# Optimization experiments

Hardware: AMD Instinct MI355X
Metric: run time of the kernel (lower is better)

Reference implementation:

```python
import jax, jax.numpy as jnp
import numpy as np
from jax import lax

B, N, S, C_IN, C_OUT = 4, 16384, 4096, 256, 256


def setup_inputs() -> dict:
    key = jax.random.key(0)
    k1, k2, k3, k4 = jax.random.split(key, 4)
    xyz1 = jax.random.normal(k1, (B, 3, N), dtype=jnp.float32)
    xyz2 = jax.random.normal(k2, (B, 3, S), dtype=jnp.float32)
    points2 = jax.random.normal(k3, (B, C_IN, S), dtype=jnp.float32)
    W = jax.random.normal(k4, (C_OUT, C_IN), dtype=jnp.float32) * (1.0 / np.sqrt(C_IN))
    b = jnp.zeros((C_OUT,), dtype=jnp.float32)
    return {"xyz1": xyz1, "xyz2": xyz2, "points2": points2, "W": W, "b": b}


def reference(xyz1, xyz2, points2, W, b):
    # channel-first -> channel-last
    p1 = jnp.transpose(xyz1, (0, 2, 1))        # [B, N, 3]
    p2 = jnp.transpose(xyz2, (0, 2, 1))        # [B, S, 3]
    f2 = jnp.transpose(points2, (0, 2, 1))     # [B, S, C]
    Bn, Nn, _ = p1.shape
    Cn = f2.shape[-1]
    # squared pairwise distances [B, N, S]
    d = (-2.0 * jnp.einsum('bnc,bsc->bns', p1, p2)
         + jnp.sum(p1 * p1, axis=-1)[:, :, None]
         + jnp.sum(p2 * p2, axis=-1)[:, None, :])
    # 3 nearest neighbors (smallest distances) -- equivalent to sort + slice :3
    neg_d3, idx = lax.top_k(-d, 3)             # [B, N, 3]
    d3 = -neg_d3
    recip = 1.0 / (d3 + 1e-8)
    weight = recip / jnp.sum(recip, axis=-1, keepdims=True)   # [B, N, 3]
    # gather neighbor features: [B, N, 3, C]
    gathered = jnp.take_along_axis(
        f2, idx.reshape(Bn, Nn * 3)[..., None], axis=1
    ).reshape(Bn, Nn, 3, Cn)
    interp = jnp.sum(gathered * weight[..., None], axis=2)    # [B, N, C]
    # Conv1d(kernel=1) == per-point linear: [B, C_out, N]
    out = jnp.einsum('bnc,oc->bon', interp, W) + b[None, :, None]
    return out
```

## Files before the change

### kernel.cpp

```cpp
#include <hip/hip_runtime.h>

#define BB 4
#define NN 16384
#define SS 4096
#define CIN 256
#define COUT 256

#define SC 8
#define SCS (SS / SC)
#define SUBS 16
#define SUBL 256
#define KNNB ((NN / 512) * SC * BB)
#define GEMMB ((COUT / 64) * (SS / 64) * BB)
#define RSLVB (BB * NN / 4)

typedef float v2f __attribute__((ext_vector_type(2)));
typedef float v4f __attribute__((ext_vector_type(4)));

__device__ __forceinline__ unsigned short f2bf(float f) {
    unsigned u = __float_as_uint(f);
    u += 0x7FFF + ((u >> 16) & 1);
    return (unsigned short)(u >> 16);
}
__device__ __forceinline__ float bf2f(unsigned short h) {
    return __uint_as_float((unsigned)h << 16);
}

__device__ __forceinline__ void ins_v(float e, float& a, float& b, float& c) {
    float n1 = __builtin_amdgcn_fmed3f(e, a, b);
    float n2 = __builtin_amdgcn_fmed3f(e, b, c);
    a = fminf(a, e); b = n1; c = n2;
}

__device__ __forceinline__ void insert_vi(float e, int gi,
                                          float& k0, float& k1, float& k2,
                                          int& i0, int& i1, int& i2) {
    bool c0 = e < k0, c1 = e < k1, c2 = e < k2;
    float n0 = fminf(e, k0);
    float n1 = __builtin_amdgcn_fmed3f(e, k0, k1);
    float n2 = __builtin_amdgcn_fmed3f(e, k1, k2);
    int t1 = c0 ? i0 : gi;
    int t2 = c1 ? i1 : gi;
    i0 = c0 ? gi : i0;
    i1 = c1 ? t1 : i1;
    i2 = c2 ? t2 : i2;
    k0 = n0; k1 = n1; k2 = n2;
}

__device__ __forceinline__ void ins_lex(float e, int gi,
                                        float& k0, float& k1, float& k2,
                                        int& i0, int& i1, int& i2) {
    bool c0 = (e < k0) || (e == k0 && gi < i0);
    bool c1 = (e < k1) || (e == k1 && gi < i1);
    bool c2 = (e < k2) || (e == k2 && gi < i2);
    float n0 = fminf(e, k0);
    float n1 = __builtin_amdgcn_fmed3f(e, k0, k1);
    float n2 = __builtin_amdgcn_fmed3f(e, k1, k2);
    int t1 = c0 ? i0 : gi;
    int t2 = c1 ? i1 : gi;
    i0 = c0 ? gi : i0;
    i1 = c1 ? t1 : i1;
    i2 = c2 ? t2 : i2;
    k0 = n0; k1 = n1; k2 = n2;
}

__device__ __forceinline__ int ltc(unsigned long long m) {
    return __builtin_amdgcn_mbcnt_hi(
        (unsigned)(m >> 32), __builtin_amdgcn_mbcnt_lo((unsigned)m, 0));
}

#define E2_FROM(p_xy, p_zw, XX, YY, ZZ, e2)                                    \
    do {                                                                       \
        asm("v_pk_fma_f32 %0, %1, %2, %3 op_sel:[0,0,1] op_sel_hi:[0,1,1]"     \
            : "=v"(e2) : "v"(p_zw), "v"(ZZ), "v"(p_zw));                       \
        asm("v_pk_fma_f32 %0, %1, %2, %0 op_sel:[1,0,0] op_sel_hi:[1,1,1]"     \
            : "+v"(e2) : "v"(p_xy), "v"(YY));                                  \
        asm("v_pk_fma_f32 %0, %1, %2, %0 op_sel:[0,0,0] op_sel_hi:[0,1,1]"     \
            : "+v"(e2) : "v"(p_xy), "v"(XX));                                  \
    } while (0)

#define PK_LO(acc, ap, bw)                                                     \
    asm("v_pk_fma_f32 %0, %1, %2, %0 op_sel:[0,0,0] op_sel_hi:[0,1,1]"         \
        : "+v"(acc) : "v"(ap), "v"(bw))
#define PK_HI(acc, ap, bw)                                                     \
    asm("v_pk_fma_f32 %0, %1, %2, %0 op_sel:[1,0,0] op_sel_hi:[1,1,1]"         \
        : "+v"(acc) : "v"(ap), "v"(bw))

__device__ __forceinline__ void knn_phase(int id, int t, float* smem,
                                          const float* __restrict__ xyz1,
                                          const float* __restrict__ xyz2,
                                          float* __restrict__ pv,
                                          float4* __restrict__ cand4) {
    int nb = id & 31;
    int ch = (id >> 5) & 7;
    int b  = id >> 8;
    int s0 = ch * SCS;

    float4* smv = (float4*)smem;
    const float* x2 = xyz2 + (size_t)b * 3 * SS;
    for (int i = t; i < SCS; i += 256) {
        float px = x2[s0 + i];
        float py = x2[SS + s0 + i];
        float pz = x2[2 * SS + s0 + i];
        float4 p4 = make_float4(px, py, pz, fmaf(px, px, fmaf(py, py, pz * pz)));
        smv[i] = p4;
        if (nb == 0) cand4[(size_t)b * SS + s0 + i] = p4;
    }
    __syncthreads();

    int n0  = nb * 512 + t;
    int n1q = n0 + 256;
    const float* xb = xyz1 + (size_t)b * 3 * NN;
    float ax = xb[n0],  ay = xb[NN + n0],  az = xb[2 * NN + n0];
    float bx = xb[n1q], by = xb[NN + n1q], bz = xb[2 * NN + n1q];
    v2f XX = {-2.0f * ax, -2.0f * bx};
    v2f YY = {-2.0f * ay, -2.0f * by};
    v2f ZZ = {-2.0f * az, -2.0f * bz};

#pragma unroll
    for (int half = 0; half < 2; ++half) {
        float A0 = 1e30f, A1 = 1e30f, A2 = 1e30f;
        float B0 = 1e30f, B1 = 1e30f, B2 = 1e30f;
        int sb = half * SUBL;
#pragma unroll 8
        for (int s = sb; s < sb + SUBL; ++s) {
            v4f p = *(const v4f*)(smem + 4 * s);
            v2f pxy = __builtin_shufflevector(p, p, 0, 1);
            v2f pzw = __builtin_shufflevector(p, p, 2, 3);
            v2f e2;
            E2_FROM(pxy, pzw, XX, YY, ZZ, e2);
            float nA1 = __builtin_amdgcn_fmed3f(e2.x, A0, A1);
            float nA2 = __builtin_amdgcn_fmed3f(e2.x, A1, A2);
            A0 = fminf(A0, e2.x); A1 = nA1; A2 = nA2;
            float nB1 = __builtin_amdgcn_fmed3f(e2.y, B0, B1);
            float nB2 = __builtin_amdgcn_fmed3f(e2.y, B1, B2);
            B0 = fminf(B0, e2.y); B1 = nB1; B2 = nB2;
        }
        int sub = ch * 2 + half;
        size_t base = (size_t)(sub * BB + b) * 3;
        pv[(base + 0) * NN + n0]  = A0;
        pv[(base + 1) * NN + n0]  = A1;
        pv[(base + 2) * NN + n0]  = A2;
        pv[(base + 0) * NN + n1q] = B0;
        pv[(base + 1) * NN + n1q] = B1;
        pv[(base + 2) * NN + n1q] = B2;
    }
}

__device__ __forceinline__ void gemm_phase(int g, int t, float* smem,
                                           const float* __restrict__ P,
                                           const float* __restrict__ W,
                                           const float* __restrict__ bias,
                                           unsigned short* __restrict__ Gh) {
    int o0 = (g & 3) * 64;
    int s0 = ((g >> 2) & 63) * 64;
    int b  = g >> 8;
    float* sP = smem;
    float* sW = smem + 1024;
    int i = t & 15;
    int j = t >> 4;

    v2f acc2[4][2];
#pragma unroll
    for (int p = 0; p < 4; ++p) {
        acc2[p][0] = (v2f){0.f, 0.f};
        acc2[p][1] = (v2f){0.f, 0.f};
    }

    const float* Pb = P + (size_t)b * CIN * SS;

    for (int c0 = 0; c0 < CIN; c0 += 16) {
        __syncthreads();
        {
            int col = t & 63;
            int r0r = t >> 6;
#pragma unroll
            for (int r = 0; r < 4; ++r) {
                int row = r0r + r * 4;
                sP[row * 64 + col] = Pb[(size_t)(c0 + row) * SS + s0 + col];
            }
        }
        {
            int cc = t & 15;
            int obase = t >> 4;
#pragma unroll
            for (int r = 0; r < 4; ++r) {
                int oo = obase + 16 * r;
                sW[cc * 68 + oo] = W[(size_t)(o0 + oo) * CIN + c0 + cc];
            }
        }
        __syncthreads();

#pragma unroll
        for (int cc = 0; cc < 16; ++cc) {
            v4f a  = *(const v4f*)&sP[cc * 64 + i * 4];
            v4f bv = *(const v4f*)&sW[cc * 68 + j * 4];
            v2f a01 = __builtin_shufflevector(a, a, 0, 1);
            v2f a23 = __builtin_shufflevector(a, a, 2, 3);
            v2f b01 = __builtin_shufflevector(bv, bv, 0, 1);
            v2f b23 = __builtin_shufflevector(bv, bv, 2, 3);
            PK_LO(acc2[0][0], a01, b01); PK_LO(acc2[0][1], a01, b23);
            PK_HI(acc2[1][0], a01, b01); PK_HI(acc2[1][1], a01, b23);
            PK_LO(acc2[2][0], a23, b01); PK_LO(acc2[2][1], a23, b23);
            PK_HI(acc2[3][0], a23, b01); PK_HI(acc2[3][1], a23, b23);
        }
    }

    float b0 = bias[o0 + j * 4 + 0];
    float b1 = bias[o0 + j * 4 + 1];
    float b2 = bias[o0 + j * 4 + 2];
    float b3 = bias[o0 + j * 4 + 3];
#pragma unroll
    for (int p = 0; p < 4; ++p) {
        ushort4 v;
        v.x = f2bf(acc2[p][0].x + b0);
        v.y = f2bf(acc2[p][0].y + b1);
        v.z = f2bf(acc2[p][1].x + b2);
        v.w = f2bf(acc2[p][1].y + b3);
        size_t off = ((size_t)b * SS + s0 + i * 4 + p) * COUT + o0 + j * 4;
        *(ushort4*)&Gh[off] = v;
    }
}

__global__ __launch_bounds__(256) void k_fused(const float* __restrict__ xyz1,
                                               const float* __restrict__ xyz2,
                                               const float* __restrict__ P,
                                               const float* __restrict__ W,
                                               const float* __restrict__ bias,
                                               unsigned short* __restrict__ Gh,
                                               float* __restrict__ pv,
                                               float4* __restrict__ cand4) {
    __shared__ float smem[2112];
    int bid = blockIdx.x;
    int t   = threadIdx.x;

    if (bid < KNNB) {
        knn_phase(bid, t, smem, xyz1, xyz2, pv, cand4);
    } else {
        gemm_phase(bid - KNNB, t, smem, P, W, bias, Gh);
    }
}

__global__ __launch_bounds__(256) void k_resolve(const float* __restrict__ pv,
                                                 const float* __restrict__ xyz1,
                                                 const float4* __restrict__ cand4,
                                                 float4* __restrict__ wi4,
                                                 int4* __restrict__ gi4) {
    __shared__ uint2 sl[4][16];
    int t   = threadIdx.x;
    int wid = t >> 6;
    int l   = t & 63;
    int g   = blockIdx.x * 4 + wid;
    int b   = g >> 14;
    int n   = g & (NN - 1);

    float ov = 1e30f;
    if (l < 48)
        ov = pv[(size_t)(((l & 15) * BB + b) * 3 + (l >> 4)) * NN + n];
    float m0 = ov, m1 = 1e30f, m2 = 1e30f;
#pragma unroll
    for (int xm = 1; xm < 64; xm <<= 1) {
        float s0 = __shfl_xor(m0, xm);
        float s1 = __shfl_xor(m1, xm);
        float s2 = __shfl_xor(m2, xm);
        ins_v(s0, m0, m1, m2);
        ins_v(s1, m0, m1, m2);
        ins_v(s2, m0, m1, m2);
    }

    unsigned mm = (unsigned)__ballot((l < 16) && (ov <= m2)) & 0xFFFFu;

    const float* xb = xyz1 + (size_t)b * 3 * NN;
    float qx = xb[n], qy = xb[NN + n], qz = xb[2 * NN + n];
    float xm2c = -2.0f * qx, ym2c = -2.0f * qy, zm2c = -2.0f * qz;
    const float4* cb = cand4 + (size_t)b * SS;

    float k0 = 1e30f, k1 = 1e30f, k2 = 1e30f;
    int   i0 = 0,     i1 = 0,     i2 = 0;
    unsigned msc = mm;
    while (msc) {
        int sub = __builtin_ctz(msc); msc &= msc - 1;
        int sb = sub * SUBL;
#pragma unroll
        for (int r = 0; r < 4; ++r) {
            int gi = sb + r * 64 + l;
            float4 p = cb[gi];
            float e = fmaf(p.x, xm2c, fmaf(p.y, ym2c, fmaf(p.z, zm2c, p.w)));
            insert_vi(e, gi, k0, k1, k2, i0, i1, i2);
        }
    }

    unsigned long long b0 = __ballot(k0 <= m2);
    unsigned long long b1 = __ballot(k1 <= m2);
    unsigned long long b2 = __ballot(k2 <= m2);
    int p0 = __popcll(b0), p1 = __popcll(b1);
    int cnt3 = p0 + p1 + __popcll(b2);
    if (cnt3 <= 16) {
        if (k0 <= m2) sl[wid][ltc(b0)]           = make_uint2(__float_as_uint(k0), (unsigned)i0);
        if (k1 <= m2) sl[wid][p0 + ltc(b1)]      = make_uint2(__float_as_uint(k1), (unsigned)i1);
        if (k2 <= m2) sl[wid][p0 + p1 + ltc(b2)] = make_uint2(__float_as_uint(k2), (unsigned)i2);
    }
    __syncthreads();

    float K0 = 1e30f, K1 = 1e30f, K2 = 1e30f;
    int   I0 = 0,     I1 = 0,     I2 = 0;
    if (cnt3 <= 16) {
        for (int j = 0; j < cnt3; ++j) {
            uint2 u = sl[wid][j];
            ins_lex(__uint_as_float(u.x), (int)u.y, K0, K1, K2, I0, I1, I2);
        }
    } else {
        unsigned mf = mm;
        while (mf) {
            int sub = __builtin_ctz(mf); mf &= mf - 1;
            int sb = sub * SUBL;
            for (int s = 0; s < SUBL; ++s) {
                float4 p = cb[sb + s];
                float e = fmaf(p.x, xm2c, fmaf(p.y, ym2c, fmaf(p.z, zm2c, p.w)));
                ins_lex(e, sb + s, K0, K1, K2, I0, I1, I2);
            }
        }
    }

    if (l == 0) {
        float nrm = fmaf(qx, qx, fmaf(qy, qy, qz * qz));
        float d0 = K0 + nrm, d1 = K1 + nrm, d2 = K2 + nrm;
        float r0 = 1.0f / (d0 + 1e-8f);
        float r1 = 1.0f / (d1 + 1e-8f);
        float r2 = 1.0f / (d2 + 1e-8f);
        float inv = 1.0f / (r0 + r1 + r2);
        size_t oq = (size_t)b * NN + n;
        wi4[oq] = make_float4(r0 * inv, r1 * inv, r2 * inv, 0.f);
        gi4[oq] = make_int4(I0, I1, I2, 0);
    }
}

__global__ __launch_bounds__(256) void k_out(const unsigned short* __restrict__ Gh,
                                             const float4* __restrict__ wi4,
                                             const int4* __restrict__ gi4,
                                             float* __restrict__ out) {
    __shared__ float  tile[64 * 68];
    __shared__ float4 swv[64];
    __shared__ int4   siv[64];
    int bid  = blockIdx.x;
    int x    = bid & 7;
    int b    = x >> 1;
    int local = (bid >> 3) + (x & 1) * 512;
    int nb   = local & 255;
    int oc   = local >> 8;
    int n0   = nb * 64;
    int o0   = oc * 64;
    int t    = threadIdx.x;
    int wave = t >> 6;
    int lane = t & 63;
    int qg   = lane >> 4;
    int c16  = lane & 15;

    if (t < 64) {
        size_t q = (size_t)b * NN + n0 + t;
        swv[t] = wi4[q];
        siv[t] = gi4[q];
    }
    __syncthreads();

    const unsigned short* Gb = Gh + (size_t)b * SS * COUT;

#pragma unroll
    for (int pass = 0; pass < 4; ++pass) {
        int q = pass * 16 + wave * 4 + qg;
        float4 wv = swv[q];
        int4   iv = siv[q];
        int co = o0 + c16 * 4;
        ushort4 a0 = *(const ushort4*)(Gb + (size_t)iv.x * COUT + co);
        ushort4 a1 = *(const ushort4*)(Gb + (size_t)iv.y * COUT + co);
        ushort4 a2 = *(const ushort4*)(Gb + (size_t)iv.z * COUT + co);
        float4 v;
        v.x = fmaf(wv.x, bf2f(a0.x), fmaf(wv.y, bf2f(a1.x), wv.z * bf2f(a2.x)));
        v.y = fmaf(wv.x, bf2f(a0.y), fmaf(wv.y, bf2f(a1.y), wv.z * bf2f(a2.y)));
        v.z = fmaf(wv.x, bf2f(a0.z), fmaf(wv.y, bf2f(a1.z), wv.z * bf2f(a2.z)));
        v.w = fmaf(wv.x, bf2f(a0.w), fmaf(wv.y, bf2f(a1.w), wv.z * bf2f(a2.w)));
        *(float4*)&tile[q * 68 + c16 * 4] = v;
    }
    __syncthreads();

    float* obase = out + ((size_t)b * COUT + o0) * NN + n0 + lane;
#pragma unroll
    for (int g = 0; g < 4; ++g) {
        int c = wave * 16 + g * 4;
        float4 v = *(const float4*)&tile[lane * 68 + c];
        obase[(size_t)(c + 0) * NN] = v.x;
        obase[(size_t)(c + 1) * NN] = v.y;
        obase[(size_t)(c + 2) * NN] = v.z;
        obase[(size_t)(c + 3) * NN] = v.w;
    }
}

extern "C" void kernel_launch(void* const* d_in, const int* in_sizes, int n_in,
                              void* d_out, int out_size, void* d_ws, size_t ws_size,
                              hipStream_t stream) {
    const float* xyz1    = (const float*)d_in[0];
    const float* xyz2    = (const float*)d_in[1];
    const float* points2 = (const float*)d_in[2];
    const float* W       = (const float*)d_in[3];
    const float* bias    = (const float*)d_in[4];
    float* out = (float*)d_out;

    char* ws = (char*)d_ws;
    float*          pv  = (float*)(ws);
    unsigned short* Gh  = (unsigned short*)(ws + 12582912);
    float4*         wi4 = (float4*)(ws + 20971520);
    int4*           gi4 = (int4*)(ws + 22020096);
    float4* cand4 = (float4*)((char*)d_out + 66846720);

    k_fused<<<dim3(KNNB + GEMMB), 256, 0, stream>>>(xyz1, xyz2, points2, W, bias,
                                                    Gh, pv, cand4);
    k_resolve<<<dim3(RSLVB), 256, 0, stream>>>(pv, xyz1, cand4, wi4, gi4);
    k_out<<<dim3(4096), 256, 0, stream>>>(Gh, wi4, gi4, out);
}
```

Before: 208.8 us.

## Batch 64 queries per resolve block with coalesced partial loads and shared setup

```diff
diff --git a/kernel.cpp b/kernel.cpp
--- a/kernel.cpp
+++ b/kernel.cpp
@@ -12,7 +12,7 @@
 #define SUBL 256
 #define KNNB ((NN / 512) * SC * BB)
 #define GEMMB ((COUT / 64) * (SS / 64) * BB)
-#define RSLVB (BB * NN / 4)
+#define RSLVB (BB * NN / 64)
 
 typedef float v2f __attribute__((ext_vector_type(2)));
 typedef float v4f __attribute__((ext_vector_type(4)));
@@ -246,92 +246,120 @@
                                                  const float4* __restrict__ cand4,
                                                  float4* __restrict__ wi4,
                                                  int4* __restrict__ gi4) {
-    __shared__ uint2 sl[4][16];
+    __shared__ float    sv[4][64][3];
+    __shared__ float    sj0[16][64];
+    __shared__ float    sm2[64];
+    __shared__ unsigned smask[64];
+    __shared__ float    sq[64][4];
+    __shared__ uint2    sl[4][16];
+    int bid = blockIdx.x;
+    int b   = bid >> 8;
+    int n0  = (bid & 255) * 64;
     int t   = threadIdx.x;
-    int wid = t >> 6;
+    int w   = t >> 6;
     int l   = t & 63;
-    int g   = blockIdx.x * 4 + wid;
-    int b   = g >> 14;
-    int n   = g & (NN - 1);
-
-    float ov = 1e30f;
-    if (l < 48)
-        ov = pv[(size_t)(((l & 15) * BB + b) * 3 + (l >> 4)) * NN + n];
-    float m0 = ov, m1 = 1e30f, m2 = 1e30f;
-#pragma unroll
-    for (int xm = 1; xm < 64; xm <<= 1) {
-        float s0 = __shfl_xor(m0, xm);
-        float s1 = __shfl_xor(m1, xm);
-        float s2 = __shfl_xor(m2, xm);
-        ins_v(s0, m0, m1, m2);
-        ins_v(s1, m0, m1, m2);
-        ins_v(s2, m0, m1, m2);
-    }
-
-    unsigned mm = (unsigned)__ballot((l < 16) && (ov <= m2)) & 0xFFFFu;
 
     const float* xb = xyz1 + (size_t)b * 3 * NN;
-    float qx = xb[n], qy = xb[NN + n], qz = xb[2 * NN + n];
-    float xm2c = -2.0f * qx, ym2c = -2.0f * qy, zm2c = -2.0f * qz;
+
+    {
+        float a0 = 1e30f, a1 = 1e30f, a2 = 1e30f;
+#pragma unroll
+        for (int i = 0; i < 12; ++i) {
+            int sub = w * 4 + i / 3;
+            int j   = i % 3;
+            float v = pv[((size_t)(sub * BB + b) * 3 + j) * NN + n0 + l];
+            if (j == 0) sj0[sub][l] = v;
+            ins_v(v, a0, a1, a2);
+        }
+        sv[w][l][0] = a0; sv[w][l][1] = a1; sv[w][l][2] = a2;
+    }
+    if (w == 1) {
+        float qx = xb[n0 + l], qy = xb[NN + n0 + l], qz = xb[2 * NN + n0 + l];
+        sq[l][0] = -2.0f * qx;
+        sq[l][1] = -2.0f * qy;
+        sq[l][2] = -2.0f * qz;
+        sq[l][3] = fmaf(qx, qx, fmaf(qy, qy, qz * qz));
+    }
+    __syncthreads();
+
+    {
+        float m0 = 1e30f, m1 = 1e30f, m2 = 1e30f;
+#pragma unroll
+        for (int ww = 0; ww < 4; ++ww) {
+            ins_v(sv[ww][l][0], m0, m1, m2);
+            ins_v(sv[ww][l][1], m0, m1, m2);
+            ins_v(sv[ww][l][2], m0, m1, m2);
+        }
+        unsigned mk = 0;
+#pragma unroll
+        for (int sub = 0; sub < SUBS; ++sub)
+            mk |= (sj0[sub][l] <= m2) ? (1u << sub) : 0u;
+        if (w == 0) { sm2[l] = m2; smask[l] = mk; }
+    }
+    __syncthreads();
+
     const float4* cb = cand4 + (size_t)b * SS;
-
-    float k0 = 1e30f, k1 = 1e30f, k2 = 1e30f;
-    int   i0 = 0,     i1 = 0,     i2 = 0;
-    unsigned msc = mm;
-    while (msc) {
-        int sub = __builtin_ctz(msc); msc &= msc - 1;
-        int sb = sub * SUBL;
-#pragma unroll
-        for (int r = 0; r < 4; ++r) {
-            int gi = sb + r * 64 + l;
-            float4 p = cb[gi];
-            float e = fmaf(p.x, xm2c, fmaf(p.y, ym2c, fmaf(p.z, zm2c, p.w)));
-            insert_vi(e, gi, k0, k1, k2, i0, i1, i2);
-        }
-    }
-
-    unsigned long long b0 = __ballot(k0 <= m2);
-    unsigned long long b1 = __ballot(k1 <= m2);
-    unsigned long long b2 = __ballot(k2 <= m2);
-    int p0 = __popcll(b0), p1 = __popcll(b1);
-    int cnt3 = p0 + p1 + __popcll(b2);
-    if (cnt3 <= 16) {
-        if (k0 <= m2) sl[wid][ltc(b0)]           = make_uint2(__float_as_uint(k0), (unsigned)i0);
-        if (k1 <= m2) sl[wid][p0 + ltc(b1)]      = make_uint2(__float_as_uint(k1), (unsigned)i1);
-        if (k2 <= m2) sl[wid][p0 + p1 + ltc(b2)] = make_uint2(__float_as_uint(k2), (unsigned)i2);
-    }
-    __syncthreads();
-
-    float K0 = 1e30f, K1 = 1e30f, K2 = 1e30f;
-    int   I0 = 0,     I1 = 0,     I2 = 0;
-    if (cnt3 <= 16) {
-        for (int j = 0; j < cnt3; ++j) {
-            uint2 u = sl[wid][j];
-            ins_lex(__uint_as_float(u.x), (int)u.y, K0, K1, K2, I0, I1, I2);
-        }
-    } else {
-        unsigned mf = mm;
-        while (mf) {
-            int sub = __builtin_ctz(mf); mf &= mf - 1;
+    for (int qq = 0; qq < 16; ++qq) {
+        int q = w * 16 + qq;
+        int n = n0 + q;
+        float    m2q = sm2[q];
+        unsigned mm  = smask[q];
+        float xm2c = sq[q][0], ym2c = sq[q][1], zm2c = sq[q][2];
+
+        float k0 = 1e30f, k1 = 1e30f, k2 = 1e30f;
+        int   i0 = 0,     i1 = 0,     i2 = 0;
+        unsigned msc = mm;
+        while (msc) {
+            int sub = __builtin_ctz(msc); msc &= msc - 1;
             int sb = sub * SUBL;
-            for (int s = 0; s < SUBL; ++s) {
-                float4 p = cb[sb + s];
+#pragma unroll
+            for (int r = 0; r < 4; ++r) {
+                int gi = sb + r * 64 + l;
+                float4 p = cb[gi];
                 float e = fmaf(p.x, xm2c, fmaf(p.y, ym2c, fmaf(p.z, zm2c, p.w)));
-                ins_lex(e, sb + s, K0, K1, K2, I0, I1, I2);
+                insert_vi(e, gi, k0, k1, k2, i0, i1, i2);
             }
         }
-    }
-
-    if (l == 0) {
-        float nrm = fmaf(qx, qx, fmaf(qy, qy, qz * qz));
-        float d0 = K0 + nrm, d1 = K1 + nrm, d2 = K2 + nrm;
-        float r0 = 1.0f / (d0 + 1e-8f);
-        float r1 = 1.0f / (d1 + 1e-8f);
-        float r2 = 1.0f / (d2 + 1e-8f);
-        float inv = 1.0f / (r0 + r1 + r2);
-        size_t oq = (size_t)b * NN + n;
-        wi4[oq] = make_float4(r0 * inv, r1 * inv, r2 * inv, 0.f);
-        gi4[oq] = make_int4(I0, I1, I2, 0);
+
+        unsigned long long b0 = __ballot(k0 <= m2q);
+        unsigned long long b1 = __ballot(k1 <= m2q);
+        unsigned long long b2 = __ballot(k2 <= m2q);
+        int p0 = __popcll(b0), p1 = __popcll(b1);
+        int cnt3 = p0 + p1 + __popcll(b2);
+        float K0 = 1e30f, K1 = 1e30f, K2 = 1e30f;
+        int   I0 = 0,     I1 = 0,     I2 = 0;
+        if (cnt3 <= 16) {
+            if (k0 <= m2q) sl[w][ltc(b0)]           = make_uint2(__float_as_uint(k0), (unsigned)i0);
+            if (k1 <= m2q) sl[w][p0 + ltc(b1)]      = make_uint2(__float_as_uint(k1), (unsigned)i1);
+            if (k2 <= m2q) sl[w][p0 + p1 + ltc(b2)] = make_uint2(__float_as_uint(k2), (unsigned)i2);
+            for (int j = 0; j < cnt3; ++j) {
+                uint2 u = sl[w][j];
+                ins_lex(__uint_as_float(u.x), (int)u.y, K0, K1, K2, I0, I1, I2);
+            }
+        } else {
+            unsigned mf = mm;
+            while (mf) {
+                int sub = __builtin_ctz(mf); mf &= mf - 1;
+                int sb = sub * SUBL;
+                for (int s = 0; s < SUBL; ++s) {
+                    float4 p = cb[sb + s];
+                    float e = fmaf(p.x, xm2c, fmaf(p.y, ym2c, fmaf(p.z, zm2c, p.w)));
+                    ins_lex(e, sb + s, K0, K1, K2, I0, I1, I2);
+                }
+            }
+        }
+
+        if (l == 0) {
+            float nrm = sq[q][3];
+            float d0 = K0 + nrm, d1 = K1 + nrm, d2 = K2 + nrm;
+            float r0 = 1.0f / (d0 + 1e-8f);
+            float r1 = 1.0f / (d1 + 1e-8f);
+            float r2 = 1.0f / (d2 + 1e-8f);
+            float inv = 1.0f / (r0 + r1 + r2);
+            size_t oq = (size_t)b * NN + n;
+            wi4[oq] = make_float4(r0 * inv, r1 * inv, r2 * inv, 0.f);
+            gi4[oq] = make_int4(I0, I1, I2, 0);
+        }
     }
 }
 
```

Measured after the change: 210.4 us. About the same (+0.8%).
